# Kernel optimization log

Hardware: AMD Instinct MI355X
Metric: run time of the kernel (lower is better)

Reference implementation:

```python
import jax, jax.numpy as jnp
import numpy as np

T = 0.07  # temperature from init default


def _l2norm(x):
    return x / jnp.linalg.norm(x, axis=1, keepdims=True)


def setup_inputs() -> dict:
    key = jax.random.key(0)
    ks = jax.random.split(key, 12)
    B, D, K = 512, 128, 4096
    G = M = 131072
    return {
        "feat": jax.random.normal(ks[0], (B, D), jnp.float32),
        "label": jax.random.randint(ks[1], (B,), 0, 2),
        "out": jnp.zeros((B, K + 1), jnp.float32),   # unused by forward
        "name": jnp.arange(B),                        # unused by forward
        "y": jax.random.randint(ks[2], (B,), 0, G),   # unused by forward
        "memory_feat_gbm": jax.random.normal(ks[3], (G, D), jnp.float32),
        "memory_prob_gbm": jax.random.uniform(ks[4], (G,), jnp.float32),
        "memory_feat_mate": jax.random.normal(ks[5], (M, D), jnp.float32),
        "memory_prob_mate": jax.random.uniform(ks[6], (M,), jnp.float32),
        "idx_n_g": jax.random.randint(ks[7], (K, 1), 0, G),
        "idx_p_g": jax.random.randint(ks[8], (1, 1), 0, G // 4),
        "idx_n_m": jax.random.randint(ks[9], (K, 1), 0, M),
        "idx_p_m": jax.random.randint(ks[10], (1, 1), 0, M // 4),
    }


def reference(feat, label, out, name, y, memory_feat_gbm, memory_prob_gbm,
              memory_feat_mate, memory_prob_mate, idx_n_g, idx_p_g, idx_n_m, idx_p_m):
    # __init__ normalizes the memory banks once
    mfg = _l2norm(memory_feat_gbm)
    mfm = _l2norm(memory_feat_mate)
    feat_n = _l2norm(feat)  # [B, D]
    output_size = mfg.shape[0]

    # gather positive / negative prototypes (all rows unit-norm, so
    # cosine_similarity == dot product)
    wp_g = mfg[idx_p_g.ravel()]   # [1, D]
    wn_g = mfg[idx_n_g.ravel()]   # [K, D]
    wp_m = mfm[idx_p_m.ravel()]   # [1, D]
    wn_m = mfm[idx_n_m.ravel()]   # [K, D]

    # label==0 (gbm): pos from gbm bank, negs from mate bank; label==1 mirrored
    row_gbm = jnp.concatenate([feat_n @ wp_g.T, feat_n @ wn_m.T], axis=1)   # [B, K+1]
    row_mate = jnp.concatenate([feat_n @ wp_m.T, feat_n @ wn_g.T], axis=1)  # [B, K+1]
    sims = jnp.where((label == 0)[:, None], row_gbm, row_mate)

    # use_softmax=False path: exp(s/T) / Z with Z set from first batch (treated as constant)
    e = jnp.exp(sims / T)
    Z = jax.lax.stop_gradient(e.mean() * output_size)
    out_feature_p_n = e / Z

    # confident cluster members + current batch (data-dependent sizes; eager jax)
    mask_g = memory_prob_gbm > 0.5
    mask_m = memory_prob_mate > 0.6
    feature_clu_all = jnp.concatenate([mfg[mask_g], mfm[mask_m], feat_n], axis=0)
    gt_clu_all = jnp.concatenate([
        jnp.zeros((int(mask_g.sum()),), label.dtype),
        jnp.ones((int(mask_m.sum()),), label.dtype),
        label,
    ], axis=0)
    return out_feature_p_n, feature_clu_all, gt_clu_all
```

## Files before the change

kernel.cpp:

```cpp
#include <hip/hip_runtime.h>
#include <math.h>


#define TINV 14.2857142857142857f
#define JT 64
#define BT2 64

typedef __attribute__((ext_vector_type(8))) short bfrag;
typedef __attribute__((ext_vector_type(4))) float ffrag;
typedef __attribute__((ext_vector_type(4))) float f4v;

__device__ __forceinline__ float wredsum64(float v) {
#pragma unroll
  for (int m = 32; m > 0; m >>= 1) v += __shfl_xor(v, m, 64);
  return v;
}

__device__ __forceinline__ int wredsum64i(int v) {
#pragma unroll
  for (int m = 32; m > 0; m >>= 1) v += __shfl_xor(v, m, 64);
  return v;
}

__device__ __forceinline__ unsigned short f2bf(float x) {
  unsigned u = __float_as_uint(x);
  u += 0x7fffu + ((u >> 16) & 1u);
  return (unsigned short)(u >> 16);
}

__device__ __forceinline__ bfrag ldsread(const short* base, int row, int kb) {
  return *(const bfrag*)((const char*)base + row * 256 +
                         (kb ^ ((row & 7) << 4)));
}
__device__ __forceinline__ void ldswrite(short* base, int row, int kb,
                                         bfrag v) {
  *(bfrag*)((char*)base + row * 256 + (kb ^ ((row & 7) << 4))) = v;
}

__global__ __launch_bounds__(256) void k_stageA(
    const float* __restrict__ feat, const int* __restrict__ label,
    const float* __restrict__ mfg, const float* __restrict__ pg,
    const float* __restrict__ mfm, const float* __restrict__ pm,
    const int* __restrict__ idxpg, const int* __restrict__ idxpm,
    float* __restrict__ outp, long long cluTail, long long gtTail,
    int* __restrict__ bucket, int* __restrict__ n0p,
    int* __restrict__ cg64, int* __restrict__ cm64,
    float* __restrict__ posPartials,
    int B, int K1, int G, int M,
    int nCountBlk, int nFeatBlk, int nPosBlk) {
  int bid = blockIdx.x, t = threadIdx.x;

  if (bid < nCountBlk) {
    int i = bid * 256 + t;
    int a = (i < G) && (pg[i] > 0.5f);
    int b = (i < M) && (pm[i] > 0.6f);
    unsigned long long ba = __ballot(a), bb = __ballot(b);
    int lane = t & 63, w = t >> 6;
    if (lane == 0) {
      cg64[bid * 4 + w] = __popcll(ba);
      cm64[bid * 4 + w] = __popcll(bb);
    }
    return;
  }
  bid -= nCountBlk;

  if (bid < nFeatBlk) {
    int gid = bid * 256 + t;
    int w = gid >> 6, lane = gid & 63;
    if (w < B) {
      float2 v = ((const float2*)feat)[(long long)w * 64 + lane];
      float sq = wredsum64(v.x * v.x + v.y * v.y);
      float inv = rsqrtf(sq);
      ((float2*)(outp + cluTail))[(long long)w * 64 + lane] =
          make_float2(v.x * inv, v.y * inv);
      if (lane == 0) outp[gtTail + w] = (float)label[w];
    }
    return;
  }
  bid -= nFeatBlk;

  if (bid < nPosBlk) {
    __shared__ float ps[4];
    int gid = bid * 256 + t;
    int w = gid >> 6, lane = gid & 63, lw = t >> 6;
    float e = 0.f;
    if (w < B) {
      int lab = label[w];
      const float* bank = lab ? mfm : mfg;
      long long row = lab ? idxpm[0] : idxpg[0];
      float2 wv = ((const float2*)(bank + row * 128))[lane];
      float2 fv = ((const float2*)feat)[(long long)w * 64 + lane];
      float dot = wredsum64(fv.x * wv.x + fv.y * wv.y);
      float sqw = wredsum64(wv.x * wv.x + wv.y * wv.y);
      float sqf = wredsum64(fv.x * fv.x + fv.y * fv.y);
      e = expf(dot * rsqrtf(sqw) * rsqrtf(sqf) * TINV);
      if (lane == 0) outp[(long long)w * K1] = e;
    }
    if (lane == 0) ps[lw] = e;
    __syncthreads();
    if (t == 0) posPartials[bid] = ps[0] + ps[1] + ps[2] + ps[3];
    return;
  }

  {
    __shared__ int sc[512];
    int t2 = t + 256;
    int m0 = (t < B) ? (label[t] == 0 ? 1 : 0) : 0;
    int m1 = (t2 < B) ? (label[t2] == 0 ? 1 : 0) : 0;
    sc[t] = m0; sc[t2] = m1;
    __syncthreads();
    for (int off = 1; off < 512; off <<= 1) {
      int u0 = (t >= off) ? sc[t - off] : 0;
      int u1 = (t2 >= off) ? sc[t2 - off] : 0;
      __syncthreads();
      sc[t] += u0; sc[t2] += u1;
      __syncthreads();
    }
    int n0 = (B > 0) ? sc[B - 1] : 0;
    if (t < B) {
      int incl = sc[t];
      if (m0) bucket[incl - 1] = t; else bucket[n0 + t - incl] = t;
    }
    if (t2 < B) {
      int incl = sc[t2];
      if (m1) bucket[incl - 1] = t2; else bucket[n0 + t2 - incl] = t2;
    }
    if (t == 0) *n0p = n0;
  }
}

__global__ __launch_bounds__(256) void k_stageB(
    const float* __restrict__ featn, const int* __restrict__ bucket,
    const int* __restrict__ n0ptr,
    const float* __restrict__ mfg, const float* __restrict__ mfm,
    const int* __restrict__ idxng, const int* __restrict__ idxnm,
    float* __restrict__ out0, float* __restrict__ partials,
    int B, int K, int K1, int simsGx) {
  __shared__ __align__(16) short wlds[64 * 128];
  __shared__ __align__(16) short flds[64 * 128];
  __shared__ float invw[64];
  __shared__ float bs[4];
  int t = threadIdx.x;
  int pidx = (int)blockIdx.x;
  int bx = pidx % simsGx, by = pidx / simsGx;
  int n0 = *n0ptr;
  int nb0 = (n0 + BT2 - 1) / BT2;
  int lab, p0, cnt;
  if (by < nb0) {
    lab = 0; p0 = by * BT2; cnt = min(BT2, n0 - p0);
  } else {
    int k = by - nb0; p0 = n0 + k * BT2;
    int n1 = B - n0; cnt = min(BT2, n1 - k * BT2); lab = 1;
  }
  if (cnt <= 0) { if (t == 0) partials[pidx] = 0.f; return; }
  const float* bank = lab == 0 ? mfm : mfg;
  const int* idxN   = lab == 0 ? idxnm : idxng;
  int j0 = bx * JT;

#pragma unroll
  for (int q = 0; q < 4; q++) {
    int slot = q * 256 + t;
    int row = slot >> 4, ch = slot & 15;
    long long srow = idxN[j0 + row];
    const float4* gp = (const float4*)(bank + srow * 128 + ch * 8);
    float4 x0 = gp[0], x1 = gp[1];
    bfrag h;
    h[0] = (short)f2bf(x0.x); h[1] = (short)f2bf(x0.y);
    h[2] = (short)f2bf(x0.z); h[3] = (short)f2bf(x0.w);
    h[4] = (short)f2bf(x1.x); h[5] = (short)f2bf(x1.y);
    h[6] = (short)f2bf(x1.z); h[7] = (short)f2bf(x1.w);
    ldswrite(wlds, row, ch * 16, h);
    float s = x0.x*x0.x + x0.y*x0.y + x0.z*x0.z + x0.w*x0.w +
              x1.x*x1.x + x1.y*x1.y + x1.z*x1.z + x1.w*x1.w;
    s += __shfl_xor(s, 1, 64);
    s += __shfl_xor(s, 2, 64);
    s += __shfl_xor(s, 4, 64);
    s += __shfl_xor(s, 8, 64);
    if (ch == 0) invw[row] = rsqrtf(s);
  }
#pragma unroll
  for (int q = 0; q < 4; q++) {
    int slot = q * 256 + t;
    int row = slot >> 4, ch = slot & 15;
    bfrag h;
#pragma unroll
    for (int i = 0; i < 8; i++) h[i] = 0;
    if (row < cnt) {
      int bg = bucket[p0 + row];
      const float4* gp = (const float4*)(featn + (long long)bg * 128 + ch * 8);
      float4 x0 = gp[0], x1 = gp[1];
      h[0] = (short)f2bf(x0.x); h[1] = (short)f2bf(x0.y);
      h[2] = (short)f2bf(x0.z); h[3] = (short)f2bf(x0.w);
      h[4] = (short)f2bf(x1.x); h[5] = (short)f2bf(x1.y);
      h[6] = (short)f2bf(x1.z); h[7] = (short)f2bf(x1.w);
    }
    ldswrite(flds, row, ch * 16, h);
  }
  __syncthreads();

  int l = t & 63, wv = t >> 6;
  int wj = wv & 1, wb = wv >> 1;
  int colb = l & 15, kg = l >> 4;
  ffrag acc00 = {0.f, 0.f, 0.f, 0.f};
  ffrag acc01 = {0.f, 0.f, 0.f, 0.f};
  ffrag acc10 = {0.f, 0.f, 0.f, 0.f};
  ffrag acc11 = {0.f, 0.f, 0.f, 0.f};
#pragma unroll
  for (int ks = 0; ks < 4; ks++) {
    int kb = ks * 64 + kg * 16;
    bfrag a0 = ldsread(flds, wb * 32 + colb,      kb);
    bfrag a1 = ldsread(flds, wb * 32 + 16 + colb, kb);
    bfrag b0 = ldsread(wlds, wj * 32 + colb,      kb);
    bfrag b1 = ldsread(wlds, wj * 32 + 16 + colb, kb);
    acc00 = __builtin_amdgcn_mfma_f32_16x16x32_bf16(a0, b0, acc00, 0, 0, 0);
    acc01 = __builtin_amdgcn_mfma_f32_16x16x32_bf16(a0, b1, acc01, 0, 0, 0);
    acc10 = __builtin_amdgcn_mfma_f32_16x16x32_bf16(a1, b0, acc10, 0, 0, 0);
    acc11 = __builtin_amdgcn_mfma_f32_16x16x32_bf16(a1, b1, acc11, 0, 0, 0);
  }

  float mysum = 0.f;
  int rowg = l >> 4;
  auto epi = [&](const ffrag& A, int bt, int jt) {
    int bl = wb * 32 + bt * 16 + rowg * 4;
    int jl = wj * 32 + jt * 16 + colb;
    float iw = invw[jl];
#pragma unroll
    for (int r = 0; r < 4; r++) {
      int b2 = bl + r;
      if (b2 < cnt) {
        int bg = bucket[p0 + b2];
        float e = expf(A[r] * iw * TINV);
        out0[(long long)bg * K1 + 1 + j0 + jl] = e;
        mysum += e;
      }
    }
  };
  epi(acc00, 0, 0); epi(acc01, 0, 1); epi(acc10, 1, 0); epi(acc11, 1, 1);

  float wsum = wredsum64(mysum);
  if ((t & 63) == 0) bs[t >> 6] = wsum;
  __syncthreads();
  if (t == 0) partials[pidx] = bs[0] + bs[1] + bs[2] + bs[3];
}

__global__ __launch_bounds__(256) void k_stageD(
    const float* __restrict__ mfg, const float* __restrict__ mfm,
    const float* __restrict__ pg, const float* __restrict__ pm,
    const int* __restrict__ cg64, const int* __restrict__ cm64,
    float* __restrict__ outp, long long cluBase, long long gtBase,
    int G, int M, int NG64, int nGatherBlk,
    float* __restrict__ out0, const float* __restrict__ partials, int nPart,
    double factor, long long n4) {
  int t = threadIdx.x;

  if ((int)blockIdx.x < nGatherBlk) {
    __shared__ float rowbuf[64][132];
    __shared__ float psum[64][33];
    __shared__ float invw[64];
    __shared__ int selRow[64];
    __shared__ int red[4];
    __shared__ int Ssh;
    int bid = blockIdx.x;
    int bankId = bid / NG64;
    int g = bid - bankId * NG64;
    const float* probs = bankId ? pm : pg;
    const float* rows  = bankId ? mfm : mfg;
    float thr = bankId ? 0.6f : 0.5f;
    int Nelem = bankId ? M : G;
    int lane = t & 63, w = t >> 6;

    int s = 0;
    for (int j = t; j < NG64; j += 256) {
      if (bankId == 0) {
        if (j < g) s += cg64[j];
      } else {
        s += cg64[j];
        if (j < g) s += cm64[j];
      }
    }
    s = wredsum64i(s);
    if (lane == 0) red[w] = s;

    if (t < 64) {
      int c = g * 64 + t;
      int f = (c < Nelem) && (probs[c] > thr);
      unsigned long long mb = __ballot(f);
      unsigned long long below = t ? ((~0ull) >> (64 - t)) : 0ull;
      if (f) selRow[__popcll(mb & below)] = c;
      if (t == 0) Ssh = (int)__popcll(mb);
    }
    __syncthreads();
    int S = Ssh;
    if (S == 0) return;
    long long off = (long long)red[0] + red[1] + red[2] + red[3];
    float labv = (float)bankId;
    int hw = t >> 5, l = t & 31;

    for (int r0 = hw * 4; r0 < S; r0 += 32) {
      int ra = r0;
      int rb = min(r0 + 1, S - 1);
      int rc = min(r0 + 2, S - 1);
      int rd = min(r0 + 3, S - 1);
      f4v v0 = *(const f4v*)(rows + (long long)selRow[ra] * 128 + l * 4);
      f4v v1 = *(const f4v*)(rows + (long long)selRow[rb] * 128 + l * 4);
      f4v v2 = *(const f4v*)(rows + (long long)selRow[rc] * 128 + l * 4);
      f4v v3 = *(const f4v*)(rows + (long long)selRow[rd] * 128 + l * 4);
      *(f4v*)&rowbuf[ra][l * 4] = v0;
      psum[ra][l] = v0.x * v0.x + v0.y * v0.y + v0.z * v0.z + v0.w * v0.w;
      *(f4v*)&rowbuf[rb][l * 4] = v1;
      psum[rb][l] = v1.x * v1.x + v1.y * v1.y + v1.z * v1.z + v1.w * v1.w;
      *(f4v*)&rowbuf[rc][l * 4] = v2;
      psum[rc][l] = v2.x * v2.x + v2.y * v2.y + v2.z * v2.z + v2.w * v2.w;
      *(f4v*)&rowbuf[rd][l * 4] = v3;
      psum[rd][l] = v3.x * v3.x + v3.y * v3.y + v3.z * v3.z + v3.w * v3.w;
    }
    __syncthreads();

    if (t < 64 && t < S) {
      float ss = 0.f;
#pragma unroll
      for (int i = 0; i < 32; i++) ss += psum[t][i];
      invw[t] = rsqrtf(ss);
    }
    __syncthreads();

    for (int r0 = hw * 4; r0 < S; r0 += 32) {
#pragma unroll
      for (int k = 0; k < 4; k++) {
        int r = r0 + k;
        if (r < S) {
          f4v v = *(const f4v*)&rowbuf[r][l * 4];
          float iw = invw[r];
          v.x *= iw; v.y *= iw; v.z *= iw; v.w *= iw;
          long long d = off + r;
          __builtin_nontemporal_store(
              v, (f4v*)(outp + cluBase + d * 128 + l * 4));
          if (l == 0)
            __builtin_nontemporal_store(labv, outp + gtBase + d);
        }
      }
    }
    return;
  }

  __shared__ double sd[256];
  double s = 0.0;
  for (int i = t; i < nPart; i += 256) s += (double)partials[i];
  sd[t] = s;
  __syncthreads();
  for (int off = 128; off > 0; off >>= 1) {
    if (t < off) sd[t] += sd[t + off];
    __syncthreads();
  }
  float sc = (float)(factor / sd[0]);
  long long base = (long long)((int)blockIdx.x - nGatherBlk) * 256 + t;
  long long stride = (long long)(gridDim.x - nGatherBlk) * 256;
  for (long long i = base; i < n4; i += stride) {
    float4 v = ((float4*)out0)[i];
    v.x *= sc; v.y *= sc; v.z *= sc; v.w *= sc;
    ((float4*)out0)[i] = v;
  }
}

extern "C" void kernel_launch(void* const* d_in, const int* in_sizes, int n_in,
                              void* d_out, int out_size, void* d_ws,
                              size_t ws_size, hipStream_t stream) {
  const float* feat  = (const float*)d_in[0];
  const int*   label = (const int*)d_in[1];
  const float* mfg   = (const float*)d_in[5];
  const float* pg    = (const float*)d_in[6];
  const float* mfm   = (const float*)d_in[7];
  const float* pm    = (const float*)d_in[8];
  const int*   idxng = (const int*)d_in[9];
  const int*   idxpg = (const int*)d_in[10];
  const int*   idxnm = (const int*)d_in[11];
  const int*   idxpm = (const int*)d_in[12];
  float* outp = (float*)d_out;

  const int B = in_sizes[1];
  const int D = 128;
  const int K = in_sizes[9];
  const int G = in_sizes[6];
  const int M = in_sizes[8];
  const int K1 = K + 1;

  const long long C0 = (long long)B * K1;
  const long long R = ((long long)out_size - C0) / (D + 1);
  const long long G0 = C0 + R * D;
  const long long cluTail = C0 + (R - B) * (long long)D;
  const long long gtTail = G0 + (R - B);

  const float* featn = outp + cluTail;

  char* wsb = (char*)d_ws;
  size_t o = 0;
  auto alloc = [&](size_t bytes) -> char* {
    char* p = wsb + o;
    o = (o + bytes + 255) & ~(size_t)255;
    return p;
  };
  const int simsGx = K / JT;
  const int simsGy = B / BT2 + 2;
  const int nPartSims = simsGx * simsGy;
  const int nPosBlk = (B * 64 + 255) / 256;
  float* partials = (float*)alloc(sizeof(float) * (nPartSims + nPosBlk));
  int* bucket = (int*)alloc(sizeof(int) * B);
  int* n0p = (int*)alloc(sizeof(int) * 4);
  const int NB = ((G > M ? G : M) + 255) / 256;
  const int NG64 = NB * 4;
  int* cg64 = (int*)alloc(sizeof(int) * NG64);
  int* cm64 = (int*)alloc(sizeof(int) * NG64);
  (void)ws_size; (void)n_in;

  const int nFeatBlk = (B * 64 + 255) / 256;
  const int gridA = NB + nFeatBlk + nPosBlk + 1;
  const int gridB = nPartSims;
  const int nGatherBlk = 2 * NG64;
  const int nScaleBlk = 1024;
  const int gridD = nGatherBlk + nScaleBlk;

  k_stageA<<<gridA, 256, 0, stream>>>(
      feat, label, mfg, pg, mfm, pm, idxpg, idxpm,
      outp, cluTail, gtTail, bucket, n0p, cg64, cm64,
      partials + nPartSims, B, K1, G, M, NB, nFeatBlk, nPosBlk);

  k_stageB<<<gridB, 256, 0, stream>>>(
      featn, bucket, n0p, mfg, mfm, idxng, idxnm,
      outp, partials, B, K, K1, simsGx);

  double factor = (double)B * (double)K1 / (double)G;
  k_stageD<<<gridD, 256, 0, stream>>>(
      mfg, mfm, pg, pm, cg64, cm64, outp, C0, G0, G, M, NG64, nGatherBlk,
      outp, partials, nPartSims + nPosBlk, factor, C0 / 4);
}
```

Measured before the change: 54.23 us.

## Compact selected row indices in stage B, gather dense row list in stage D

The mask scan and prefix offset computation move from the gather blocks in stage D into extra blocks of stage B. Those blocks write a compact list of selected rows, with the bank id packed into the upper bits, and they also write the gt labels. Stage D then launches one block per 32 selected rows, so it no longer launches one block per 64-element chunk that is mostly empty, and it drops the LDS staging by normalizing through wave shuffles. The number of scale blocks is halved and nontemporal stores are removed. In exchange this adds a workspace buffer, and the rowlist writes go through global memory between the two launches.

```diff
diff --git a/kernel.cpp b/kernel.cpp
--- a/kernel.cpp
+++ b/kernel.cpp
@@ -133,14 +133,55 @@
     const float* __restrict__ featn, const int* __restrict__ bucket,
     const int* __restrict__ n0ptr,
     const float* __restrict__ mfg, const float* __restrict__ mfm,
+    const float* __restrict__ pg, const float* __restrict__ pm,
     const int* __restrict__ idxng, const int* __restrict__ idxnm,
+    const int* __restrict__ cg64, const int* __restrict__ cm64,
     float* __restrict__ out0, float* __restrict__ partials,
-    int B, int K, int K1, int simsGx) {
+    int* __restrict__ rowlist, float* __restrict__ outp, long long gtBase,
+    int B, int K, int K1, int G, int M, int NG64, int simsGx, int nSimsBlk) {
+  int t = threadIdx.x;
+
+  if ((int)blockIdx.x >= nSimsBlk) {
+    __shared__ int red[4];
+    int gb = (int)blockIdx.x - nSimsBlk;
+    int bankId = gb / NG64;
+    int g = gb - bankId * NG64;
+    const float* probs = bankId ? pm : pg;
+    float thr = bankId ? 0.6f : 0.5f;
+    int Nelem = bankId ? M : G;
+    int lane = t & 63, w = t >> 6;
+
+    int s = 0;
+    for (int j = t; j < NG64; j += 256) {
+      if (bankId == 0) {
+        if (j < g) s += cg64[j];
+      } else {
+        s += cg64[j];
+        if (j < g) s += cm64[j];
+      }
+    }
+    s = wredsum64i(s);
+    if (lane == 0) red[w] = s;
+    __syncthreads();
+    if (t < 64) {
+      long long off = (long long)red[0] + red[1] + red[2] + red[3];
+      int c = g * 64 + t;
+      int f = (c < Nelem) && (probs[c] > thr);
+      unsigned long long mb = __ballot(f);
+      unsigned long long below = t ? ((~0ull) >> (64 - t)) : 0ull;
+      if (f) {
+        long long dst = off + __popcll(mb & below);
+        rowlist[dst] = c | (bankId << 24);
+        outp[gtBase + dst] = (float)bankId;
+      }
+    }
+    return;
+  }
+
   __shared__ __align__(16) short wlds[64 * 128];
   __shared__ __align__(16) short flds[64 * 128];
   __shared__ float invw[64];
   __shared__ float bs[4];
-  int t = threadIdx.x;
   int pidx = (int)blockIdx.x;
   int bx = pidx % simsGx, by = pidx / simsGx;
   int n0 = *n0ptr;
@@ -245,98 +286,47 @@
 
 __global__ __launch_bounds__(256) void k_stageD(
     const float* __restrict__ mfg, const float* __restrict__ mfm,
-    const float* __restrict__ pg, const float* __restrict__ pm,
-    const int* __restrict__ cg64, const int* __restrict__ cm64,
-    float* __restrict__ outp, long long cluBase, long long gtBase,
-    int G, int M, int NG64, int nGatherBlk,
+    const int* __restrict__ rowlist,
+    float* __restrict__ outp, long long cluBase, int nSel, int nGatherBlk,
     float* __restrict__ out0, const float* __restrict__ partials, int nPart,
     double factor, long long n4) {
   int t = threadIdx.x;
 
   if ((int)blockIdx.x < nGatherBlk) {
-    __shared__ float rowbuf[64][132];
-    __shared__ float psum[64][33];
-    __shared__ float invw[64];
-    __shared__ int selRow[64];
-    __shared__ int red[4];
-    __shared__ int Ssh;
-    int bid = blockIdx.x;
-    int bankId = bid / NG64;
-    int g = bid - bankId * NG64;
-    const float* probs = bankId ? pm : pg;
-    const float* rows  = bankId ? mfm : mfg;
-    float thr = bankId ? 0.6f : 0.5f;
-    int Nelem = bankId ? M : G;
-    int lane = t & 63, w = t >> 6;
-
-    int s = 0;
-    for (int j = t; j < NG64; j += 256) {
-      if (bankId == 0) {
-        if (j < g) s += cg64[j];
-      } else {
-        s += cg64[j];
-        if (j < g) s += cm64[j];
-      }
-    }
-    s = wredsum64i(s);
-    if (lane == 0) red[w] = s;
-
-    if (t < 64) {
-      int c = g * 64 + t;
-      int f = (c < Nelem) && (probs[c] > thr);
-      unsigned long long mb = __ballot(f);
-      unsigned long long below = t ? ((~0ull) >> (64 - t)) : 0ull;
-      if (f) selRow[__popcll(mb & below)] = c;
-      if (t == 0) Ssh = (int)__popcll(mb);
+    __shared__ int rl[32];
+    int base = (int)blockIdx.x * 32;
+    if (t < 32) {
+      int d = base + t;
+      rl[t] = (d < nSel) ? rowlist[d] : 0;
     }
     __syncthreads();
-    int S = Ssh;
-    if (S == 0) return;
-    long long off = (long long)red[0] + red[1] + red[2] + red[3];
-    float labv = (float)bankId;
     int hw = t >> 5, l = t & 31;
-
-    for (int r0 = hw * 4; r0 < S; r0 += 32) {
-      int ra = r0;
-      int rb = min(r0 + 1, S - 1);
-      int rc = min(r0 + 2, S - 1);
-      int rd = min(r0 + 3, S - 1);
-      f4v v0 = *(const f4v*)(rows + (long long)selRow[ra] * 128 + l * 4);
-      f4v v1 = *(const f4v*)(rows + (long long)selRow[rb] * 128 + l * 4);
-      f4v v2 = *(const f4v*)(rows + (long long)selRow[rc] * 128 + l * 4);
-      f4v v3 = *(const f4v*)(rows + (long long)selRow[rd] * 128 + l * 4);
-      *(f4v*)&rowbuf[ra][l * 4] = v0;
-      psum[ra][l] = v0.x * v0.x + v0.y * v0.y + v0.z * v0.z + v0.w * v0.w;
-      *(f4v*)&rowbuf[rb][l * 4] = v1;
-      psum[rb][l] = v1.x * v1.x + v1.y * v1.y + v1.z * v1.z + v1.w * v1.w;
-      *(f4v*)&rowbuf[rc][l * 4] = v2;
-      psum[rc][l] = v2.x * v2.x + v2.y * v2.y + v2.z * v2.z + v2.w * v2.w;
-      *(f4v*)&rowbuf[rd][l * 4] = v3;
-      psum[rd][l] = v3.x * v3.x + v3.y * v3.y + v3.z * v3.z + v3.w * v3.w;
-    }
-    __syncthreads();
-
-    if (t < 64 && t < S) {
-      float ss = 0.f;
-#pragma unroll
-      for (int i = 0; i < 32; i++) ss += psum[t][i];
-      invw[t] = rsqrtf(ss);
-    }
-    __syncthreads();
-
-    for (int r0 = hw * 4; r0 < S; r0 += 32) {
-#pragma unroll
-      for (int k = 0; k < 4; k++) {
-        int r = r0 + k;
-        if (r < S) {
-          f4v v = *(const f4v*)&rowbuf[r][l * 4];
-          float iw = invw[r];
-          v.x *= iw; v.y *= iw; v.z *= iw; v.w *= iw;
-          long long d = off + r;
-          __builtin_nontemporal_store(
-              v, (f4v*)(outp + cluBase + d * 128 + l * 4));
-          if (l == 0)
-            __builtin_nontemporal_store(labv, outp + gtBase + d);
+#pragma unroll
+    for (int k = 0; k < 2; k++) {
+      int r0 = hw * 4 + k * 2, r1 = r0 + 1;
+      if (base + r0 < nSel) {
+        bool h1 = (base + r1) < nSel;
+        int e0 = rl[r0];
+        int e1 = rl[h1 ? r1 : r0];
+        const float* p0 = ((e0 >> 24) ? mfm : mfg) +
+                          (long long)(e0 & 0xFFFFFF) * 128;
+        const float* p1 = ((e1 >> 24) ? mfm : mfg) +
+                          (long long)(e1 & 0xFFFFFF) * 128;
+        f4v v0 = *(const f4v*)(p0 + l * 4);
+        f4v v1 = *(const f4v*)(p1 + l * 4);
+        float q0 = v0.x * v0.x + v0.y * v0.y + v0.z * v0.z + v0.w * v0.w;
+        float q1 = v1.x * v1.x + v1.y * v1.y + v1.z * v1.z + v1.w * v1.w;
+#pragma unroll
+        for (int m = 16; m > 0; m >>= 1) {
+          q0 += __shfl_xor(q0, m, 64);
+          q1 += __shfl_xor(q1, m, 64);
+        }
+        float i0 = rsqrtf(q0), i1 = rsqrtf(q1);
+        f4v o0 = {v0.x * i0, v0.y * i0, v0.z * i0, v0.w * i0};
+        *(f4v*)(outp + cluBase + (long long)(base + r0) * 128 + l * 4) = o0;
+        if (h1) {
+          f4v o1 = {v1.x * i1, v1.y * i1, v1.z * i1, v1.w * i1};
+          *(f4v*)(outp + cluBase + (long long)(base + r1) * 128 + l * 4) = o1;
         }
       }
     }
@@ -353,9 +343,9 @@
     __syncthreads();
   }
   float sc = (float)(factor / sd[0]);
-  long long base = (long long)((int)blockIdx.x - nGatherBlk) * 256 + t;
+  long long bb = (long long)((int)blockIdx.x - nGatherBlk) * 256 + t;
   long long stride = (long long)(gridDim.x - nGatherBlk) * 256;
-  for (long long i = base; i < n4; i += stride) {
+  for (long long i = bb; i < n4; i += stride) {
     float4 v = ((float4*)out0)[i];
     v.x *= sc; v.y *= sc; v.z *= sc; v.w *= sc;
     ((float4*)out0)[i] = v;
@@ -389,6 +379,7 @@
   const long long G0 = C0 + R * D;
   const long long cluTail = C0 + (R - B) * (long long)D;
   const long long gtTail = G0 + (R - B);
+  const int nSel = (int)(R - B);
 
   const float* featn = outp + cluTail;
 
@@ -410,13 +401,15 @@
   const int NG64 = NB * 4;
   int* cg64 = (int*)alloc(sizeof(int) * NG64);
   int* cm64 = (int*)alloc(sizeof(int) * NG64);
+  int* rowlist = (int*)alloc(sizeof(int) * (size_t)nSel);
   (void)ws_size; (void)n_in;
 
   const int nFeatBlk = (B * 64 + 255) / 256;
   const int gridA = NB + nFeatBlk + nPosBlk + 1;
-  const int gridB = nPartSims;
-  const int nGatherBlk = 2 * NG64;
-  const int nScaleBlk = 1024;
+  const int nEmitBlk = 2 * NG64;
+  const int gridB = nPartSims + nEmitBlk;
+  const int nGatherBlk = (nSel + 31) / 32;
+  const int nScaleBlk = 512;
   const int gridD = nGatherBlk + nScaleBlk;
 
   k_stageA<<<gridA, 256, 0, stream>>>(
@@ -425,11 +418,12 @@
       partials + nPartSims, B, K1, G, M, NB, nFeatBlk, nPosBlk);
 
   k_stageB<<<gridB, 256, 0, stream>>>(
-      featn, bucket, n0p, mfg, mfm, idxng, idxnm,
-      outp, partials, B, K, K1, simsGx);
+      featn, bucket, n0p, mfg, mfm, pg, pm, idxng, idxnm,
+      cg64, cm64, outp, partials, rowlist, outp, G0,
+      B, K, K1, G, M, NG64, simsGx, nPartSims);
 
   double factor = (double)B * (double)K1 / (double)G;
   k_stageD<<<gridD, 256, 0, stream>>>(
-      mfg, mfm, pg, pm, cg64, cm64, outp, C0, G0, G, M, NG64, nGatherBlk,
+      mfg, mfm, rowlist, outp, C0, nSel, nGatherBlk,
       outp, partials, nPartSims + nPosBlk, factor, C0 / 4);
 }
```

Result: faster. 52.13 us (-3.9%).
